# Performance work log

Hardware: AMD Instinct MI355X
Metric: run time of the kernel (lower is better)

## Reference

```python
import jax, jax.numpy as jnp
import numpy as np

N_NODES = 100000
N_EDGES = 1600000
D_IN, D_HID, D_OUT = 128, 256, 128


def _sage_conv(x, src, dst, W_l, b_l, W_r, num_nodes):
    """PyG SAGEConv with mean aggregation: lin_l(mean_j x_j) + lin_r(x_i)."""
    msg = x[src]                                              # [E, d] gather
    agg = jax.ops.segment_sum(msg, dst, num_segments=num_nodes)   # [N, d]
    cnt = jax.ops.segment_sum(jnp.ones((src.shape[0],), x.dtype), dst,
                              num_segments=num_nodes)         # [N]
    agg = agg / jnp.maximum(cnt, 1.0)[:, None]                # mean (0 for isolated)
    return agg @ W_l + b_l + x @ W_r


def setup_inputs() -> dict:
    key = jax.random.key(0)
    ks = jax.random.split(key, 8)
    x = jax.random.normal(ks[0], (N_NODES, D_IN), dtype=jnp.float32)
    edge_index = jax.random.randint(ks[1], (2, N_EDGES), 0, N_NODES, dtype=jnp.int64)
    perturb_first = jax.random.normal(ks[2], (N_NODES, D_HID), dtype=jnp.float32) * 0.05
    perturb_last = jax.random.normal(ks[3], (N_NODES, D_OUT), dtype=jnp.float32) * 0.05
    s1 = 1.0 / np.sqrt(D_IN)
    s2 = 1.0 / np.sqrt(D_HID)
    return {
        "x": x,
        "edge_index": edge_index,
        "perturb_first": perturb_first,
        "perturb_last": perturb_last,
        "Wl1": jax.random.normal(ks[4], (D_IN, D_HID), dtype=jnp.float32) * s1,
        "bl1": jnp.zeros((D_HID,), dtype=jnp.float32),
        "Wr1": jax.random.normal(ks[5], (D_IN, D_HID), dtype=jnp.float32) * s1,
        "Wl2": jax.random.normal(ks[6], (D_HID, D_OUT), dtype=jnp.float32) * s2,
        "bl2": jnp.zeros((D_OUT,), dtype=jnp.float32),
        "Wr2": jax.random.normal(ks[7], (D_HID, D_OUT), dtype=jnp.float32) * s2,
    }


def reference(x, edge_index, perturb_first, perturb_last,
              Wl1, bl1, Wr1, Wl2, bl2, Wr2):
    # PyG default flow source_to_target: messages from edge_index[0] -> edge_index[1]
    src, dst = edge_index[0], edge_index[1]
    n = x.shape[0]
    # forward() only applies model[0] and model[3] (the two SAGEConvs);
    # the LayerNorm/PReLU entries in the Sequential are skipped.
    h = _sage_conv(x, src, dst, Wl1, bl1, Wr1, n) + perturb_first
    out = _sage_conv(h, src, dst, Wl2, bl2, Wr2, n) + perturb_last
    return out
```

## Files before the change

kernel.cpp:

```cpp
#include <hip/hip_runtime.h>

#define N_NODES 100000
#define N_EDGES 1600000
#define NBUCK 196
#define CAP_BIN 64
#define CAP_B 12288
#define CVT_BLKS 12500

typedef float v4f __attribute__((ext_vector_type(4)));
typedef __bf16 v8bf __attribute__((ext_vector_type(8)));
typedef __bf16 v4bf __attribute__((ext_vector_type(4)));
typedef unsigned int v4u __attribute__((ext_vector_type(4)));

union FragU { v4u u; v8bf b; };
union PkU { unsigned int u; __bf16 h[2]; };
union Pk2 { uint2 u2; __bf16 h[4]; };

__device__ __forceinline__ int clampN(int v) {
    return v < 0 ? 0 : (v >= N_NODES ? N_NODES - 1 : v);
}
__device__ __forceinline__ float bfhi(unsigned int u) { return __uint_as_float(u & 0xffff0000u); }
__device__ __forceinline__ float bflo(unsigned int u) { return __uint_as_float(u << 16); }

__global__ __launch_bounds__(256) void k_prep(
    const float* __restrict__ x, __bf16* __restrict__ a2,
    const float* __restrict__ Wl1, const float* __restrict__ Wr1,
    const float* __restrict__ Wl2, const float* __restrict__ Wr2,
    __bf16* __restrict__ Wl1p, __bf16* __restrict__ Wr1p,
    __bf16* __restrict__ Wl2p, __bf16* __restrict__ Wr2p,
    const int* __restrict__ dst, int* __restrict__ bucketCnt)
{
    const int b = blockIdx.x, tid = threadIdx.x;
    if (b < CVT_BLKS) {
        int t = b * 256 + tid;
        float4 v = ((const float4*)x)[t];
        int row = t >> 5, c4 = t & 31;
        v4bf o = { (__bf16)v.x, (__bf16)v.y, (__bf16)v.z, (__bf16)v.w };
        *(v4bf*)(a2 + (size_t)row * 256 + 128 + c4 * 4) = o;
    } else if (b < CVT_BLKS + 64) {
        int pb = b - CVT_BLKS;
        int which = pb >> 4;
        int t = (pb & 15) * 256 + tid;
        const float* W = which == 0 ? Wl1 : which == 1 ? Wr1 : which == 2 ? Wl2 : Wr2;
        __bf16* Wp     = which == 0 ? Wl1p : which == 1 ? Wr1p : which == 2 ? Wl2p : Wr2p;
        const int N = (which < 2) ? 256 : 128;
        const int NT = N >> 4;
        int l = t & 63;
        int fi = t >> 6;
        int kc = fi / NT, nt = fi % NT;
        int k0 = kc * 32 + (l >> 4) * 8;
        int col = nt * 16 + (l & 15);
        v8bf o;
        #pragma unroll
        for (int j = 0; j < 8; ++j) o[j] = (__bf16)W[(size_t)(k0 + j) * N + col];
        *(v8bf*)(Wp + (size_t)t * 8) = o;
    } else {
        __shared__ int h[NBUCK];
        for (int i = tid; i < NBUCK; i += 256) h[i] = 0;
        __syncthreads();
        int cb = b - CVT_BLKS - 64;
        int e0 = cb * 4096;
        int e1 = e0 + 4096; if (e1 > N_EDGES) e1 = N_EDGES;
        for (int e = e0 + tid; e < e1; e += 256)
            atomicAdd(&h[clampN(dst[e]) >> 9], 1);
        __syncthreads();
        for (int i = tid; i < NBUCK; i += 256)
            if (h[i]) atomicAdd(&bucketCnt[i], h[i]);
    }
}

__global__ __launch_bounds__(256) void k_scanb(
    const int* __restrict__ bucketCnt, int* __restrict__ baseB,
    int* __restrict__ gcur, int* __restrict__ rowp)
{
    const int t = threadIdx.x;
    int v = (t < NBUCK) ? bucketCnt[t] : 0;
    int incl = v;
    #pragma unroll
    for (int off = 1; off < 64; off <<= 1) {
        int u = __shfl_up(incl, off);
        if ((t & 63) >= off) incl += u;
    }
    __shared__ int wt[4];
    if ((t & 63) == 63) wt[t >> 6] = incl;
    __syncthreads();
    int woff = 0;
    #pragma unroll
    for (int k = 0; k < 4; ++k) if (k < (t >> 6)) woff += wt[k];
    int excl = woff + incl - v;
    if (t < NBUCK) { baseB[t] = excl; gcur[t] = excl; }
    if (t == NBUCK) { baseB[NBUCK] = excl; rowp[N_NODES] = excl; }
}

__global__ __launch_bounds__(256) void k_bin(
    const int* __restrict__ src, const int* __restrict__ dst,
    int* __restrict__ gcur, unsigned int* __restrict__ packed)
{
    __shared__ unsigned int bins[256 * CAP_BIN];
    __shared__ int cnt[256];
    const int tid = threadIdx.x;
    cnt[tid] = 0;
    __syncthreads();
    const int epb = (N_EDGES + gridDim.x - 1) / gridDim.x;
    int e0 = blockIdx.x * epb;
    int e1 = e0 + epb; if (e1 > N_EDGES) e1 = N_EDGES;
    for (int ch = e0; ch < e1; ch += 4096) {
        int chEnd = ch + 4096; if (chEnd > e1) chEnd = e1;
        for (int e = ch + tid; e < chEnd; e += 256) {
            int s = clampN(src[e]);
            int d = clampN(dst[e]);
            unsigned int val = (unsigned int)s | ((unsigned int)(d & 511) << 17);
            int b = d >> 9;
            int slot = atomicAdd(&cnt[b], 1);
            if (slot < CAP_BIN) bins[b * CAP_BIN + slot] = val;
            else {
                int g = atomicAdd(&gcur[b], 1);
                packed[g] = val;
            }
        }
        __syncthreads();
        int n = cnt[tid]; if (n > CAP_BIN) n = CAP_BIN;
        if (tid < NBUCK && n > 0) {
            int g = atomicAdd(&gcur[tid], n);
            for (int j = 0; j < n; ++j) packed[g + j] = bins[tid * CAP_BIN + j];
        }
        __syncthreads();
        cnt[tid] = 0;
        __syncthreads();
    }
}

__global__ __launch_bounds__(256) void k_bucket(
    const int* __restrict__ baseB, const unsigned int* __restrict__ packed,
    int* __restrict__ rowp, int* __restrict__ edge_src)
{
    __shared__ int hist[512], cur[512];
    __shared__ int wt[4];
    __shared__ unsigned int buf[CAP_B];
    const int b = blockIdx.x, tid = threadIdx.x;
    const int lo = baseB[b], hi = baseB[b + 1], c = hi - lo;
    for (int i = tid; i < 512; i += 256) hist[i] = 0;
    __syncthreads();
    for (int e = tid; e < c; e += 256)
        atomicAdd(&hist[packed[lo + e] >> 17], 1);
    __syncthreads();
    int a0 = hist[2 * tid], a1 = hist[2 * tid + 1];
    int s = a0 + a1;
    int incl = s;
    #pragma unroll
    for (int off = 1; off < 64; off <<= 1) {
        int u = __shfl_up(incl, off);
        if ((tid & 63) >= off) incl += u;
    }
    if ((tid & 63) == 63) wt[tid >> 6] = incl;
    __syncthreads();
    int woff = 0;
    #pragma unroll
    for (int k = 0; k < 4; ++k) if (k < (tid >> 6)) woff += wt[k];
    int ep = woff + incl - s;
    cur[2 * tid] = ep;
    cur[2 * tid + 1] = ep + a0;
    int n0 = b * 512 + 2 * tid;
    if (n0 < N_NODES)     rowp[n0]     = lo + ep;
    if (n0 + 1 < N_NODES) rowp[n0 + 1] = lo + ep + a0;
    __syncthreads();
    for (int e = tid; e < c; e += 256) {
        unsigned int v = packed[lo + e];
        int dl = v >> 17;
        unsigned int sv = v & 0x1FFFFu;
        int pos = atomicAdd(&cur[dl], 1);
        if (pos < CAP_B) buf[pos] = sv;
        else edge_src[lo + pos] = (int)sv;
    }
    __syncthreads();
    int cc = c < CAP_B ? c : CAP_B;
    for (int e = tid; e < cc; e += 256) edge_src[lo + e] = (int)buf[e];
}

template<int MODE>
__global__ __launch_bounds__(256) void k_gather16(
    const int* __restrict__ rp, const int* __restrict__ es,
    const __bf16* __restrict__ tab, void* __restrict__ outp)
{
    int wid = (blockIdx.x * 256 + threadIdx.x) >> 6;
    int l = threadIdx.x & 63;
    if (wid >= N_NODES) return;
    int start = rp[wid], end = rp[wid + 1];
    const int slot = l >> 4, c = l & 15;
    const size_t coff = (MODE == 0) ? (size_t)(128 + c * 8) : (size_t)(c * 8);
    float s0 = 0.f, s1 = 0.f, s2 = 0.f, s3 = 0.f;
    float s4 = 0.f, s5 = 0.f, s6 = 0.f, s7 = 0.f;

    int e0 = start + slot;
    int e1 = e0 + 4;
    int e2 = e1 + 4;
    bool h0 = e0 < end, h1 = e1 < end, h2 = e2 < end;
    v4u r0 = {0, 0, 0, 0}, r1 = {0, 0, 0, 0};
    if (h0) r0 = *(const v4u*)(tab + (size_t)es[e0] * 256 + coff);
    if (h1) r1 = *(const v4u*)(tab + (size_t)es[e1] * 256 + coff);
    int i2 = h2 ? es[e2] : 0;

    while (h0) {
        v4u r2 = {0, 0, 0, 0};
        if (h2) r2 = *(const v4u*)(tab + (size_t)i2 * 256 + coff);
        int e3 = e2 + 4;
        bool h3 = e3 < end;
        int i3 = h3 ? es[e3] : 0;
        s0 += bflo(r0.x); s1 += bfhi(r0.x);
        s2 += bflo(r0.y); s3 += bfhi(r0.y);
        s4 += bflo(r0.z); s5 += bfhi(r0.z);
        s6 += bflo(r0.w); s7 += bfhi(r0.w);
        r0 = r1; r1 = r2;
        h0 = h1; h1 = h2; h2 = h3;
        i2 = i3; e2 = e3;
    }

    s0 += __shfl_xor(s0, 16); s1 += __shfl_xor(s1, 16);
    s2 += __shfl_xor(s2, 16); s3 += __shfl_xor(s3, 16);
    s4 += __shfl_xor(s4, 16); s5 += __shfl_xor(s5, 16);
    s6 += __shfl_xor(s6, 16); s7 += __shfl_xor(s7, 16);
    s0 += __shfl_xor(s0, 32); s1 += __shfl_xor(s1, 32);
    s2 += __shfl_xor(s2, 32); s3 += __shfl_xor(s3, 32);
    s4 += __shfl_xor(s4, 32); s5 += __shfl_xor(s5, 32);
    s6 += __shfl_xor(s6, 32); s7 += __shfl_xor(s7, 32);
    float invd = 1.f / fmaxf((float)(end - start), 1.f);
    if (slot == 0) {
        if (MODE == 0) {
            PkU a, b, cc, d;
            a.h[0] = (__bf16)(s0 * invd); a.h[1] = (__bf16)(s1 * invd);
            b.h[0] = (__bf16)(s2 * invd); b.h[1] = (__bf16)(s3 * invd);
            cc.h[0] = (__bf16)(s4 * invd); cc.h[1] = (__bf16)(s5 * invd);
            d.h[0] = (__bf16)(s6 * invd); d.h[1] = (__bf16)(s7 * invd);
            v4u o = { a.u, b.u, cc.u, d.u };
            ((v4u*)outp)[(size_t)wid * 32 + c] = o;
        } else {
            v4u pu = *(const v4u*)(tab + (size_t)wid * 256 + 128 + c * 8);
            float4 va, vb;
            va.x = s0 * invd + bflo(pu.x); va.y = s1 * invd + bfhi(pu.x);
            va.z = s2 * invd + bflo(pu.y); va.w = s3 * invd + bfhi(pu.y);
            vb.x = s4 * invd + bflo(pu.z); vb.y = s5 * invd + bfhi(pu.z);
            vb.z = s6 * invd + bflo(pu.w); vb.w = s7 * invd + bfhi(pu.w);
            ((float4*)outp)[(size_t)wid * 32 + c * 2]     = va;
            ((float4*)outp)[(size_t)wid * 32 + c * 2 + 1] = vb;
        }
    }
}

__device__ __forceinline__ void ld_stage(
    const __bf16* __restrict__ A, int tile, int tid, v4u st[4])
{
    const int row0 = tile * 64;
    #pragma unroll
    for (int cc = 0; cc < 4; ++cc) {
        int chunk = cc * 512 + tid;
        int row = chunk >> 5, col16 = chunk & 31;
        st[cc] = *(const v4u*)(A + (size_t)(row0 + row) * 256 + col16 * 8);
    }
}

template<int LAYER>
__global__ __launch_bounds__(512, 2) void k_gws(
    const __bf16* __restrict__ A,
    const __bf16* __restrict__ WpA, const __bf16* __restrict__ WpB,
    const float* __restrict__ bias, const float* __restrict__ pert,
    __bf16* __restrict__ outb, int ntiles)
{
    __shared__ char aS[32768];
    __shared__ char hS[32768];
    const int tid = threadIdx.x;
    const int w = tid >> 6, l = tid & 63;
    const int lrow = l & 15, kg = l >> 4;
    const v4f zf = {0.f, 0.f, 0.f, 0.f};

    FragU bw[8][2];
    #pragma unroll
    for (int kc = 0; kc < 8; ++kc)
        #pragma unroll
        for (int nt = 0; nt < 2; ++nt) {
            const __bf16* Wp;
            int fi;
            if (LAYER == 1) {
                Wp = (kc < 4) ? WpA : WpB;
                fi = (kc & 3) * 16 + w * 2 + nt;
            } else {
                Wp = (w < 4) ? WpA : WpB;
                fi = kc * 8 + (w & 3) * 2 + nt;
            }
            bw[kc][nt].u = *(const v4u*)(Wp + ((size_t)fi * 64 + l) * 8);
        }

    int tile = blockIdx.x;
    v4u st[4];
    if (tile < ntiles) ld_stage(A, tile, tid, st);

    for (; tile < ntiles; tile += gridDim.x) {
        #pragma unroll
        for (int cc = 0; cc < 4; ++cc) {
            int chunk = cc * 512 + tid;
            int row = chunk >> 5, col16 = chunk & 31;
            int byte = (row * 512 + col16 * 16) ^ ((row & 7) << 4);
            *(v4u*)(aS + byte) = st[cc];
        }
        int nxt = tile + (int)gridDim.x;
        if (nxt < ntiles) ld_stage(A, nxt, tid, st);
        __syncthreads();

        const int row0 = tile * 64;
        #pragma unroll
        for (int rf = 0; rf < 4; ++rf) {
            const int arow = rf * 16 + lrow;
            FragU a[8];
            #pragma unroll
            for (int kc = 0; kc < 8; ++kc) {
                int byte = arow * 512 + ((kc * 64 + kg * 16) ^ ((arow & 7) << 4));
                a[kc].u = *(const v4u*)(aS + byte);
            }
            v4f acc[2] = {zf, zf};
            #pragma unroll
            for (int kc = 0; kc < 8; ++kc) {
                acc[0] = __builtin_amdgcn_mfma_f32_16x16x32_bf16(a[kc].b, bw[kc][0].b, acc[0], 0, 0, 0);
                acc[1] = __builtin_amdgcn_mfma_f32_16x16x32_bf16(a[kc].b, bw[kc][1].b, acc[1], 0, 0, 0);
            }
            #pragma unroll
            for (int nt = 0; nt < 2; ++nt)
                #pragma unroll
                for (int r = 0; r < 4; ++r) {
                    int row = rf * 16 + kg * 4 + r;
                    int col = w * 32 + nt * 16 + lrow;
                    int byte = (row * 512 + col * 2) ^ ((row & 7) << 4);
                    *(__bf16*)(hS + byte) = (__bf16)acc[nt][r];
                }
        }
        __syncthreads();

        #pragma unroll
        for (int it = 0; it < 8; ++it) {
            int chunk = it * 512 + tid;
            int row = chunk >> 6, c4 = chunk & 63;
            int grow = row0 + row;
            if (grow >= N_NODES) continue;
            int byte = (row * 512 + c4 * 8) ^ ((row & 7) << 4);
            Pk2 pk; pk.u2 = *(const uint2*)(hS + byte);
            if (LAYER == 1) {
                float4 pv = ((const float4*)pert)[(size_t)grow * 64 + c4];
                float4 bv = ((const float4*)bias)[c4];
                PkU o0, o1;
                o0.h[0] = (__bf16)((float)pk.h[0] + pv.x + bv.x);
                o0.h[1] = (__bf16)((float)pk.h[1] + pv.y + bv.y);
                o1.h[0] = (__bf16)((float)pk.h[2] + pv.z + bv.z);
                o1.h[1] = (__bf16)((float)pk.h[3] + pv.w + bv.w);
                uint2 ov = { o0.u, o1.u };
                *(uint2*)(outb + (size_t)grow * 256 + c4 * 4) = ov;
            } else {
                uint2 ov;
                if (c4 < 32) {
                    ov = pk.u2;
                } else {
                    int oc4 = c4 - 32;
                    float4 pv = ((const float4*)pert)[(size_t)grow * 32 + oc4];
                    float4 bv = ((const float4*)bias)[oc4];
                    PkU o0, o1;
                    o0.h[0] = (__bf16)((float)pk.h[0] + pv.x + bv.x);
                    o0.h[1] = (__bf16)((float)pk.h[1] + pv.y + bv.y);
                    o1.h[0] = (__bf16)((float)pk.h[2] + pv.z + bv.z);
                    o1.h[1] = (__bf16)((float)pk.h[3] + pv.w + bv.w);
                    ov.x = o0.u; ov.y = o1.u;
                }
                *(uint2*)(outb + (size_t)grow * 256 + c4 * 4) = ov;
            }
        }
    }
}

extern "C" void kernel_launch(void* const* d_in, const int* in_sizes, int n_in,
                              void* d_out, int out_size, void* d_ws, size_t ws_size,
                              hipStream_t stream)
{
    const float* x   = (const float*)d_in[0];
    const int*   ei  = (const int*)d_in[1];
    const float* p1  = (const float*)d_in[2];
    const float* p2  = (const float*)d_in[3];
    const float* Wl1 = (const float*)d_in[4];
    const float* bl1 = (const float*)d_in[5];
    const float* Wr1 = (const float*)d_in[6];
    const float* Wl2 = (const float*)d_in[7];
    const float* bl2 = (const float*)d_in[8];
    const float* Wr2 = (const float*)d_in[9];
    const int* src = ei;
    const int* dst = ei + N_EDGES;

    const size_t NPAD = (size_t)N_NODES + 64;
    char* wp = (char*)d_ws;
    __bf16* a2   = (__bf16*)wp; wp += NPAD * 256 * 2;
    __bf16* hb   = (__bf16*)wp; wp += NPAD * 256 * 2;
    __bf16* u2b  = (__bf16*)wp; wp += NPAD * 256 * 2;
    __bf16* Wl1p = (__bf16*)wp; wp += 128 * 256 * 2;
    __bf16* Wr1p = (__bf16*)wp; wp += 128 * 256 * 2;
    __bf16* Wl2p = (__bf16*)wp; wp += 256 * 128 * 2;
    __bf16* Wr2p = (__bf16*)wp; wp += 256 * 128 * 2;
    int* bucketCnt = (int*)wp; wp += 512 * 4;
    int* baseB     = (int*)wp; wp += 512 * 4;
    int* gcur      = (int*)wp; wp += 512 * 4;
    int* rowp      = (int*)wp; wp += (size_t)(N_NODES + 1) * 4 + 12;
    unsigned int* packed = (unsigned int*)wp; wp += (size_t)N_EDGES * 4;
    int* es        = (int*)wp;

    hipMemsetAsync(bucketCnt, 0, 512 * 4, stream);

    const int gblocks = (N_NODES * 64 + 255) / 256;
    const int tiles = (N_NODES + 63) / 64;
    const int prep_blocks = CVT_BLKS + 64 + (N_EDGES + 4095) / 4096;

    k_prep<<<prep_blocks, 256, 0, stream>>>(
        x, a2, Wl1, Wr1, Wl2, Wr2, Wl1p, Wr1p, Wl2p, Wr2p, dst, bucketCnt);
    k_scanb<<<1, 256, 0, stream>>>(bucketCnt, baseB, gcur, rowp);
    k_bin<<<256, 256, 0, stream>>>(src, dst, gcur, packed);
    k_bucket<<<NBUCK, 256, 0, stream>>>(baseB, packed, rowp, es);

    k_gather16<0><<<gblocks, 256, 0, stream>>>(rowp, es, a2, a2);
    k_gws<1><<<512, 512, 0, stream>>>(a2, Wl1p, Wr1p, bl1, p1, hb, tiles);
    k_gws<2><<<512, 512, 0, stream>>>(hb, Wl2p, Wr2p, bl2, p2, u2b, tiles);
    k_gather16<1><<<gblocks, 256, 0, stream>>>(rowp, es, u2b, (void*)d_out);
}
```

Baseline: 317.4 us.

## Stage GEMM weights in LDS and process independent per-wave 16-row strips

New measurement: 662.5 us. 109% more time.

```diff
diff --git a/kernel.cpp b/kernel.cpp
--- a/kernel.cpp
+++ b/kernel.cpp
@@ -14,7 +14,7 @@
 
 union FragU { v4u u; v8bf b; };
 union PkU { unsigned int u; __bf16 h[2]; };
-union Pk2 { uint2 u2; __bf16 h[4]; };
+union Pk4 { v4u u4; __bf16 h[8]; };
 
 __device__ __forceinline__ int clampN(int v) {
     return v < 0 ? 0 : (v >= N_NODES ? N_NODES - 1 : v);
@@ -246,127 +246,121 @@
     }
 }
 
-__device__ __forceinline__ void ld_stage(
-    const __bf16* __restrict__ A, int tile, int tid, v4u st[4])
-{
-    const int row0 = tile * 64;
-    #pragma unroll
-    for (int cc = 0; cc < 4; ++cc) {
-        int chunk = cc * 512 + tid;
-        int row = chunk >> 5, col16 = chunk & 31;
-        st[cc] = *(const v4u*)(A + (size_t)(row0 + row) * 256 + col16 * 8);
-    }
-}
-
 template<int LAYER>
-__global__ __launch_bounds__(512, 2) void k_gws(
+__global__ __launch_bounds__(768, 3) void k_gws(
     const __bf16* __restrict__ A,
     const __bf16* __restrict__ WpA, const __bf16* __restrict__ WpB,
     const float* __restrict__ bias, const float* __restrict__ pert,
-    __bf16* __restrict__ outb, int ntiles)
-{
-    __shared__ char aS[32768];
-    __shared__ char hS[32768];
+    __bf16* __restrict__ outb)
+{
+    __shared__ char bS[131072];
+    __shared__ char eS[12 * 2048];
     const int tid = threadIdx.x;
-    const int w = tid >> 6, l = tid & 63;
+    const int wv = tid >> 6, l = tid & 63;
     const int lrow = l & 15, kg = l >> 4;
     const v4f zf = {0.f, 0.f, 0.f, 0.f};
 
-    FragU bw[8][2];
-    #pragma unroll
-    for (int kc = 0; kc < 8; ++kc)
+    {
+        const v4u* ga = (const v4u*)WpA;
+        const v4u* gb = (const v4u*)WpB;
+        v4u* sa = (v4u*)bS;
+        v4u* sb = (v4u*)(bS + 65536);
+        for (int i = tid; i < 4096; i += 768) {
+            sa[i] = ga[i];
+            sb[i] = gb[i];
+        }
+    }
+    __syncthreads();
+
+    char* myE = eS + wv * 2048;
+    const int nstrips = N_NODES / 16;
+    const int stride = gridDim.x * 12;
+
+    for (int strip = blockIdx.x * 12 + wv; strip < nstrips; strip += stride) {
+        const int rowbase = strip * 16;
+        const int arow = rowbase + lrow;
+
+        FragU a[8];
         #pragma unroll
-        for (int nt = 0; nt < 2; ++nt) {
-            const __bf16* Wp;
-            int fi;
-            if (LAYER == 1) {
-                Wp = (kc < 4) ? WpA : WpB;
-                fi = (kc & 3) * 16 + w * 2 + nt;
-            } else {
-                Wp = (w < 4) ? WpA : WpB;
-                fi = kc * 8 + (w & 3) * 2 + nt;
-            }
-            bw[kc][nt].u = *(const v4u*)(Wp + ((size_t)fi * 64 + l) * 8);
-        }
-
-    int tile = blockIdx.x;
-    v4u st[4];
-    if (tile < ntiles) ld_stage(A, tile, tid, st);
-
-    for (; tile < ntiles; tile += gridDim.x) {
+        for (int kc = 0; kc < 8; ++kc)
+            a[kc].u = *(const v4u*)(A + (size_t)arow * 256 + kc * 32 + kg * 8);
+
         #pragma unroll
-        for (int cc = 0; cc < 4; ++cc) {
-            int chunk = cc * 512 + tid;
-            int row = chunk >> 5, col16 = chunk & 31;
-            int byte = (row * 512 + col16 * 16) ^ ((row & 7) << 4);
-            *(v4u*)(aS + byte) = st[cc];
-        }
-        int nxt = tile + (int)gridDim.x;
-        if (nxt < ntiles) ld_stage(A, nxt, tid, st);
-        __syncthreads();
-
-        const int row0 = tile * 64;
-        #pragma unroll
-        for (int rf = 0; rf < 4; ++rf) {
-            const int arow = rf * 16 + lrow;
-            FragU a[8];
+        for (int p = 0; p < 2; ++p) {
+            v4f acc[8];
+            #pragma unroll
+            for (int nt = 0; nt < 8; ++nt) acc[nt] = zf;
             #pragma unroll
             for (int kc = 0; kc < 8; ++kc) {
-                int byte = arow * 512 + ((kc * 64 + kg * 16) ^ ((arow & 7) << 4));
-                a[kc].u = *(const v4u*)(aS + byte);
-            }
-            v4f acc[2] = {zf, zf};
-            #pragma unroll
-            for (int kc = 0; kc < 8; ++kc) {
-                acc[0] = __builtin_amdgcn_mfma_f32_16x16x32_bf16(a[kc].b, bw[kc][0].b, acc[0], 0, 0, 0);
-                acc[1] = __builtin_amdgcn_mfma_f32_16x16x32_bf16(a[kc].b, bw[kc][1].b, acc[1], 0, 0, 0);
+                #pragma unroll
+                for (int nt = 0; nt < 8; ++nt) {
+                    const int ntg = p * 8 + nt;
+                    size_t boff;
+                    if (LAYER == 1) {
+                        boff = (kc < 4)
+                            ? ((size_t)((kc * 16 + ntg) * 64 + l)) * 16
+                            : 65536u + ((size_t)(((kc - 4) * 16 + ntg) * 64 + l)) * 16;
+                    } else {
+                        boff = (ntg < 8)
+                            ? ((size_t)((kc * 8 + ntg) * 64 + l)) * 16
+                            : 65536u + ((size_t)((kc * 8 + (ntg - 8)) * 64 + l)) * 16;
+                    }
+                    FragU bf_; bf_.u = *(const v4u*)(bS + boff);
+                    acc[nt] = __builtin_amdgcn_mfma_f32_16x16x32_bf16(a[kc].b, bf_.b, acc[nt], 0, 0, 0);
+                }
             }
             #pragma unroll
-            for (int nt = 0; nt < 2; ++nt)
+            for (int q = 0; q < 2; ++q) {
                 #pragma unroll
-                for (int r = 0; r < 4; ++r) {
-                    int row = rf * 16 + kg * 4 + r;
-                    int col = w * 32 + nt * 16 + lrow;
-                    int byte = (row * 512 + col * 2) ^ ((row & 7) << 4);
-                    *(__bf16*)(hS + byte) = (__bf16)acc[nt][r];
+                for (int nt = 0; nt < 4; ++nt)
+                    #pragma unroll
+                    for (int r = 0; r < 4; ++r) {
+                        int row = kg * 4 + r;
+                        int off = (nt * 32 + lrow * 2) ^ ((row & 7) << 4);
+                        *(__bf16*)(myE + row * 128 + off) = (__bf16)acc[q * 4 + nt][r];
+                    }
+                const int row = l >> 2, cq = l & 3;
+                const int off0 = (cq * 32) ^ ((row & 7) << 4);
+                const int off1 = (cq * 32 + 16) ^ ((row & 7) << 4);
+                Pk4 lo, hi;
+                lo.u4 = *(const v4u*)(myE + row * 128 + off0);
+                hi.u4 = *(const v4u*)(myE + row * 128 + off1);
+                const int grow = rowbase + row;
+                const int colb = p * 128 + q * 64 + cq * 16;
+                if (LAYER == 1 || p == 1) {
+                    const int pcolb = (LAYER == 1) ? colb : (colb - 128);
+                    const int pstride = (LAYER == 1) ? 64 : 32;
+                    float4 pv0 = ((const float4*)pert)[(size_t)grow * pstride + (pcolb >> 2)];
+                    float4 pv1 = ((const float4*)pert)[(size_t)grow * pstride + (pcolb >> 2) + 1];
+                    float4 pv2 = ((const float4*)pert)[(size_t)grow * pstride + (pcolb >> 2) + 2];
+                    float4 pv3 = ((const float4*)pert)[(size_t)grow * pstride + (pcolb >> 2) + 3];
+                    float4 bv0 = ((const float4*)bias)[(pcolb >> 2)];
+                    float4 bv1 = ((const float4*)bias)[(pcolb >> 2) + 1];
+                    float4 bv2 = ((const float4*)bias)[(pcolb >> 2) + 2];
+                    float4 bv3 = ((const float4*)bias)[(pcolb >> 2) + 3];
+                    Pk4 o0, o1;
+                    o0.h[0] = (__bf16)((float)lo.h[0] + pv0.x + bv0.x);
+                    o0.h[1] = (__bf16)((float)lo.h[1] + pv0.y + bv0.y);
+                    o0.h[2] = (__bf16)((float)lo.h[2] + pv0.z + bv0.z);
+                    o0.h[3] = (__bf16)((float)lo.h[3] + pv0.w + bv0.w);
+                    o0.h[4] = (__bf16)((float)lo.h[4] + pv1.x + bv1.x);
+                    o0.h[5] = (__bf16)((float)lo.h[5] + pv1.y + bv1.y);
+                    o0.h[6] = (__bf16)((float)lo.h[6] + pv1.z + bv1.z);
+                    o0.h[7] = (__bf16)((float)lo.h[7] + pv1.w + bv1.w);
+                    o1.h[0] = (__bf16)((float)hi.h[0] + pv2.x + bv2.x);
+                    o1.h[1] = (__bf16)((float)hi.h[1] + pv2.y + bv2.y);
+                    o1.h[2] = (__bf16)((float)hi.h[2] + pv2.z + bv2.z);
+                    o1.h[3] = (__bf16)((float)hi.h[3] + pv2.w + bv2.w);
+                    o1.h[4] = (__bf16)((float)hi.h[4] + pv3.x + bv3.x);
+                    o1.h[5] = (__bf16)((float)hi.h[5] + pv3.y + bv3.y);
+                    o1.h[6] = (__bf16)((float)hi.h[6] + pv3.z + bv3.z);
+                    o1.h[7] = (__bf16)((float)hi.h[7] + pv3.w + bv3.w);
+                    *(v4u*)(outb + (size_t)grow * 256 + colb)     = o0.u4;
+                    *(v4u*)(outb + (size_t)grow * 256 + colb + 8) = o1.u4;
+                } else {
+                    *(v4u*)(outb + (size_t)grow * 256 + colb)     = lo.u4;
+                    *(v4u*)(outb + (size_t)grow * 256 + colb + 8) = hi.u4;
                 }
-        }
-        __syncthreads();
-
-        #pragma unroll
-        for (int it = 0; it < 8; ++it) {
-            int chunk = it * 512 + tid;
-            int row = chunk >> 6, c4 = chunk & 63;
-            int grow = row0 + row;
-            if (grow >= N_NODES) continue;
-            int byte = (row * 512 + c4 * 8) ^ ((row & 7) << 4);
-            Pk2 pk; pk.u2 = *(const uint2*)(hS + byte);
-            if (LAYER == 1) {
-                float4 pv = ((const float4*)pert)[(size_t)grow * 64 + c4];
-                float4 bv = ((const float4*)bias)[c4];
-                PkU o0, o1;
-                o0.h[0] = (__bf16)((float)pk.h[0] + pv.x + bv.x);
-                o0.h[1] = (__bf16)((float)pk.h[1] + pv.y + bv.y);
-                o1.h[0] = (__bf16)((float)pk.h[2] + pv.z + bv.z);
-                o1.h[1] = (__bf16)((float)pk.h[3] + pv.w + bv.w);
-                uint2 ov = { o0.u, o1.u };
-                *(uint2*)(outb + (size_t)grow * 256 + c4 * 4) = ov;
-            } else {
-                uint2 ov;
-                if (c4 < 32) {
-                    ov = pk.u2;
-                } else {
-                    int oc4 = c4 - 32;
-                    float4 pv = ((const float4*)pert)[(size_t)grow * 32 + oc4];
-                    float4 bv = ((const float4*)bias)[oc4];
-                    PkU o0, o1;
-                    o0.h[0] = (__bf16)((float)pk.h[0] + pv.x + bv.x);
-                    o0.h[1] = (__bf16)((float)pk.h[1] + pv.y + bv.y);
-                    o1.h[0] = (__bf16)((float)pk.h[2] + pv.z + bv.z);
-                    o1.h[1] = (__bf16)((float)pk.h[3] + pv.w + bv.w);
-                    ov.x = o0.u; ov.y = o1.u;
-                }
-                *(uint2*)(outb + (size_t)grow * 256 + c4 * 4) = ov;
             }
         }
     }
@@ -408,7 +402,6 @@
     hipMemsetAsync(bucketCnt, 0, 512 * 4, stream);
 
     const int gblocks = (N_NODES * 64 + 255) / 256;
-    const int tiles = (N_NODES + 63) / 64;
     const int prep_blocks = CVT_BLKS + 64 + (N_EDGES + 4095) / 4096;
 
     k_prep<<<prep_blocks, 256, 0, stream>>>(
@@ -418,7 +411,7 @@
     k_bucket<<<NBUCK, 256, 0, stream>>>(baseB, packed, rowp, es);
 
     k_gather16<0><<<gblocks, 256, 0, stream>>>(rowp, es, a2, a2);
-    k_gws<1><<<512, 512, 0, stream>>>(a2, Wl1p, Wr1p, bl1, p1, hb, tiles);
-    k_gws<2><<<512, 512, 0, stream>>>(hb, Wl2p, Wr2p, bl2, p2, u2b, tiles);
+    k_gws<1><<<256, 768, 0, stream>>>(a2, Wl1p, Wr1p, bl1, p1, hb);
+    k_gws<2><<<256, 768, 0, stream>>>(hb, Wl2p, Wr2p, bl2, p2, u2b);
     k_gather16<1><<<gblocks, 256, 0, stream>>>(rowp, es, u2b, (void*)d_out);
 }
```

## Double-buffer GEMM A tiles via direct global-to-LDS loads and stage perturbation

Applied to the files above, without the earlier changes.

Measured after the change: 289.4 us, median of 2. 8.8% less time.

```diff
diff --git a/kernel.cpp b/kernel.cpp
--- a/kernel.cpp
+++ b/kernel.cpp
@@ -21,6 +21,12 @@
 }
 __device__ __forceinline__ float bfhi(unsigned int u) { return __uint_as_float(u & 0xffff0000u); }
 __device__ __forceinline__ float bflo(unsigned int u) { return __uint_as_float(u << 16); }
+
+__device__ __forceinline__ void gll16(const void* g, void* l) {
+    __builtin_amdgcn_global_load_lds(
+        (const __attribute__((address_space(1))) unsigned int*)g,
+        (__attribute__((address_space(3))) unsigned int*)l, 16, 0, 0);
+}
 
 __global__ __launch_bounds__(256) void k_prep(
     const float* __restrict__ x, __bf16* __restrict__ a2,
@@ -246,15 +252,39 @@
     }
 }
 
-__device__ __forceinline__ void ld_stage(
-    const __bf16* __restrict__ A, int tile, int tid, v4u st[4])
-{
-    const int row0 = tile * 64;
-    #pragma unroll
-    for (int cc = 0; cc < 4; ++cc) {
-        int chunk = cc * 512 + tid;
-        int row = chunk >> 5, col16 = chunk & 31;
-        st[cc] = *(const v4u*)(A + (size_t)(row0 + row) * 256 + col16 * 8);
+template<int LAYER>
+__device__ __forceinline__ void stage_a32(
+    const __bf16* __restrict__ A, int tile, int tid, char* buf)
+{
+    const int row0 = tile * 32;
+    #pragma unroll
+    for (int k = 0; k < 2; ++k) {
+        int ch = k * 512 + tid;
+        int row = ch >> 5, c16 = ch & 31;
+        int sc = c16 ^ (row & 7);
+        gll16(A + (size_t)(row0 + row) * 256 + sc * 8, buf + ch * 16);
+    }
+}
+
+template<int LAYER>
+__device__ __forceinline__ void stage_p32(
+    const float* __restrict__ pert, int tile, int tid, char* pS)
+{
+    const int row0 = tile * 32;
+    if (LAYER == 1) {
+        #pragma unroll
+        for (int k = 0; k < 4; ++k) {
+            int ch = k * 512 + tid;
+            int row = ch >> 6, c16 = ch & 63;
+            gll16(pert + (size_t)(row0 + row) * 256 + c16 * 4, pS + ch * 16);
+        }
+    } else {
+        #pragma unroll
+        for (int k = 0; k < 2; ++k) {
+            int ch = k * 512 + tid;
+            int row = ch >> 5, c16 = ch & 31;
+            gll16(pert + (size_t)(row0 + row) * 128 + c16 * 4, pS + ch * 16);
+        }
     }
 }
 
@@ -265,8 +295,10 @@
     const float* __restrict__ bias, const float* __restrict__ pert,
     __bf16* __restrict__ outb, int ntiles)
 {
-    __shared__ char aS[32768];
-    __shared__ char hS[32768];
+    __shared__ char aS0[16384];
+    __shared__ char aS1[16384];
+    __shared__ char hS[16384];
+    __shared__ char pS[(LAYER == 1) ? 32768 : 16384];
     const int tid = threadIdx.x;
     const int w = tid >> 6, l = tid & 63;
     const int lrow = l & 15, kg = l >> 4;
@@ -290,30 +322,26 @@
         }
 
     int tile = blockIdx.x;
-    v4u st[4];
-    if (tile < ntiles) ld_stage(A, tile, tid, st);
+    int cur = 0;
+    if (tile < ntiles) stage_a32<LAYER>(A, tile, tid, aS0);
+    __syncthreads();
 
     for (; tile < ntiles; tile += gridDim.x) {
-        #pragma unroll
-        for (int cc = 0; cc < 4; ++cc) {
-            int chunk = cc * 512 + tid;
-            int row = chunk >> 5, col16 = chunk & 31;
-            int byte = (row * 512 + col16 * 16) ^ ((row & 7) << 4);
-            *(v4u*)(aS + byte) = st[cc];
-        }
+        stage_p32<LAYER>(pert, tile, tid, pS);
         int nxt = tile + (int)gridDim.x;
-        if (nxt < ntiles) ld_stage(A, nxt, tid, st);
-        __syncthreads();
-
-        const int row0 = tile * 64;
-        #pragma unroll
-        for (int rf = 0; rf < 4; ++rf) {
+        if (nxt < ntiles)
+            stage_a32<LAYER>(A, nxt, tid, cur ? aS0 : aS1);
+        const char* aSc = cur ? aS1 : aS0;
+
+        const int row0 = tile * 32;
+        #pragma unroll
+        for (int rf = 0; rf < 2; ++rf) {
             const int arow = rf * 16 + lrow;
             FragU a[8];
             #pragma unroll
             for (int kc = 0; kc < 8; ++kc) {
                 int byte = arow * 512 + ((kc * 64 + kg * 16) ^ ((arow & 7) << 4));
-                a[kc].u = *(const v4u*)(aS + byte);
+                a[kc].u = *(const v4u*)(aSc + byte);
             }
             v4f acc[2] = {zf, zf};
             #pragma unroll
@@ -334,15 +362,14 @@
         __syncthreads();
 
         #pragma unroll
-        for (int it = 0; it < 8; ++it) {
+        for (int it = 0; it < 4; ++it) {
             int chunk = it * 512 + tid;
             int row = chunk >> 6, c4 = chunk & 63;
             int grow = row0 + row;
-            if (grow >= N_NODES) continue;
             int byte = (row * 512 + c4 * 8) ^ ((row & 7) << 4);
             Pk2 pk; pk.u2 = *(const uint2*)(hS + byte);
             if (LAYER == 1) {
-                float4 pv = ((const float4*)pert)[(size_t)grow * 64 + c4];
+                float4 pv = *(const float4*)(pS + (row * 64 + c4) * 16);
                 float4 bv = ((const float4*)bias)[c4];
                 PkU o0, o1;
                 o0.h[0] = (__bf16)((float)pk.h[0] + pv.x + bv.x);
@@ -356,9 +383,8 @@
                 if (c4 < 32) {
                     ov = pk.u2;
                 } else {
-                    int oc4 = c4 - 32;
-                    float4 pv = ((const float4*)pert)[(size_t)grow * 32 + oc4];
-                    float4 bv = ((const float4*)bias)[oc4];
+                    float4 pv = *(const float4*)(pS + (row * 32 + (c4 - 32)) * 16);
+                    float4 bv = ((const float4*)bias)[c4 - 32];
                     PkU o0, o1;
                     o0.h[0] = (__bf16)((float)pk.h[0] + pv.x + bv.x);
                     o0.h[1] = (__bf16)((float)pk.h[1] + pv.y + bv.y);
@@ -369,6 +395,8 @@
                 *(uint2*)(outb + (size_t)grow * 256 + c4 * 4) = ov;
             }
         }
+        __syncthreads();
+        cur ^= 1;
     }
 }
 
@@ -408,7 +436,7 @@
     hipMemsetAsync(bucketCnt, 0, 512 * 4, stream);
 
     const int gblocks = (N_NODES * 64 + 255) / 256;
-    const int tiles = (N_NODES + 63) / 64;
+    const int tiles32 = N_NODES / 32;
     const int prep_blocks = CVT_BLKS + 64 + (N_EDGES + 4095) / 4096;
 
     k_prep<<<prep_blocks, 256, 0, stream>>>(
@@ -418,7 +446,7 @@
     k_bucket<<<NBUCK, 256, 0, stream>>>(baseB, packed, rowp, es);
 
     k_gather16<0><<<gblocks, 256, 0, stream>>>(rowp, es, a2, a2);
-    k_gws<1><<<512, 512, 0, stream>>>(a2, Wl1p, Wr1p, bl1, p1, hb, tiles);
-    k_gws<2><<<512, 512, 0, stream>>>(hb, Wl2p, Wr2p, bl2, p2, u2b, tiles);
+    k_gws<1><<<512, 512, 0, stream>>>(a2, Wl1p, Wr1p, bl1, p1, hb, tiles32);
+    k_gws<2><<<512, 512, 0, stream>>>(hb, Wl2p, Wr2p, bl2, p2, u2b, tiles32);
     k_gather16<1><<<gblocks, 256, 0, stream>>>(rowp, es, u2b, (void*)d_out);
 }
```
